# Kernel tuning notes

Hardware: AMD Instinct MI355X
Metric: run time of the kernel (lower is better)

Reference implementation:

```python
import jax, jax.numpy as jnp
import numpy as np

D_IN = 128      # NODE/EDGE_EMBEDDING_SIZE
FC_HID = 512    # FC_HIDDEN_SIZE
FEAT = 256      # GNN_FEAT_SIZE
N1 = 2000; E1 = 2000; N2 = 2000; E2 = 2000
GNN_LAYERS = 3
ALPHA = 200.0   # NORM_ALPHA
BS_ITERS = 10   # BS_ITER_NUM
BS_EPS = 1e-4   # BS_EPSILON


def _l2norm(x, axis=-1, eps=1e-12):
    # torch F.normalize(p=2): x / max(||x||, eps)
    n = jnp.sqrt(jnp.sum(x * x, axis=axis, keepdims=True))
    return x / jnp.maximum(n, eps)


def _pairwise_sim(x, y):
    # s = 1 - cdist(x,y,p=2)/max  on batched [B,N,D],[B,M,D]
    x2 = jnp.sum(x * x, axis=-1)[:, :, None]
    y2 = jnp.sum(y * y, axis=-1)[:, None, :]
    d2 = jnp.maximum(x2 + y2 - 2.0 * jnp.einsum('bnd,bmd->bnm', x, y), 0.0)
    dist = jnp.sqrt(d2)
    return 1.0 - dist / jnp.max(dist)


def _gconv(A, x, w_a, b_a, w_u, b_u):
    # A: [B,N,N]; F.normalize(A, p=1, dim=-2) = column L1 normalization
    An = A / jnp.maximum(jnp.sum(jnp.abs(A), axis=-2, keepdims=True), 1e-12)
    ax = jax.nn.relu(x @ w_a + b_a)
    ux = jax.nn.relu(x @ w_u + b_u)
    return jnp.einsum('bnm,bmd->bnd', An, ax) + ux


def _affinity(X, Y, A):
    S = (A + A.T) * 0.5
    return jnp.einsum('bnd,de,bme->bnm', X, S, Y)


def _sinkhorn(s, n1, n2):
    # nrows/ncols equal full dims in Net.forward, so masks are full blocks.
    NT1, NT2 = s.shape[1], s.shape[2]
    r = jnp.arange(NT1)[:, None]
    c = jnp.arange(NT2)[None, :]
    block = ((r < n1) & (c < n2)) | ((r >= n1) & (c >= n2))
    s = (s + BS_EPS) * block[None].astype(s.dtype)
    for i in range(BS_ITERS):
        if i % 2 == 1:
            s = s / jnp.sum(s, axis=2, keepdims=True)  # row normalization
        else:
            s = s / jnp.sum(s, axis=1, keepdims=True)  # column normalization
    return s


def setup_inputs() -> dict:
    key = jax.random.key(0)
    ks = jax.random.split(key, 22)
    f32 = jnp.float32
    def lin_w(k, din, dout):
        return jax.random.uniform(k, (din, dout), dtype=f32,
                                  minval=-1.0, maxval=1.0) / np.sqrt(din)
    stdv = 1.0 / np.sqrt(FEAT)
    inp = {
        'emb1': jax.random.normal(ks[0], (1, N1, D_IN), dtype=f32),
        'emb2': jax.random.normal(ks[1], (1, N2, D_IN), dtype=f32),
        'edge_emb1': jax.random.normal(ks[2], (1, E1, D_IN), dtype=f32),
        'edge_emb2': jax.random.normal(ks[3], (1, E2, D_IN), dtype=f32),
        'Aidx_src': jax.random.uniform(ks[4], (1, N1 + E1, N1 + E1), dtype=f32),
        'Aidx_tgt': jax.random.uniform(ks[5], (1, N2 + E2, N2 + E2), dtype=f32),
        'fc1n_w': lin_w(ks[6], D_IN, FC_HID), 'fc1n_b': jnp.zeros((FC_HID,), f32),
        'fc2n_w': lin_w(ks[7], FC_HID, FEAT), 'fc2n_b': jnp.zeros((FEAT,), f32),
        'fc1e_w': lin_w(ks[8], D_IN, FC_HID), 'fc1e_b': jnp.zeros((FC_HID,), f32),
        'fc2e_w': lin_w(ks[9], FC_HID, FEAT), 'fc2e_b': jnp.zeros((FEAT,), f32),
        'gnn_a_w': jnp.stack([lin_w(k, FEAT, FEAT) for k in jax.random.split(ks[10], GNN_LAYERS)]),
        'gnn_a_b': jnp.zeros((GNN_LAYERS, FEAT), f32),
        'gnn_u_w': jnp.stack([lin_w(k, FEAT, FEAT) for k in jax.random.split(ks[11], GNN_LAYERS)]),
        'gnn_u_b': jnp.zeros((GNN_LAYERS, FEAT), f32),
        'aff_A': jax.random.uniform(ks[12], (GNN_LAYERS, FEAT, FEAT), dtype=f32,
                                    minval=-stdv, maxval=stdv) + jnp.eye(FEAT, dtype=f32),
        'cg_w': lin_w(ks[13], 2 * FEAT, FEAT), 'cg_b': jnp.zeros((FEAT,), f32),
    }
    return inp


def reference(emb1, emb2, edge_emb1, edge_emb2, Aidx_src, Aidx_tgt,
              fc1n_w, fc1n_b, fc2n_w, fc2n_b, fc1e_w, fc1e_b, fc2e_w, fc2e_b,
              gnn_a_w, gnn_a_b, gnn_u_w, gnn_u_b, aff_A, cg_w, cg_b):
    # node embeddings
    h1 = jax.nn.relu(emb1[0] @ fc1n_w + fc1n_b)
    e1n = _l2norm(h1 @ fc2n_w + fc2n_b)[None]            # [1,N1,FEAT]
    h2 = jax.nn.relu(emb2[0] @ fc1n_w + fc1n_b)
    e2n = _l2norm(h2 @ fc2n_w + fc2n_b)[None]            # [1,N2,FEAT]
    Kp = _pairwise_sim(e1n, e2n)
    # edge embeddings
    g1 = jax.nn.relu(edge_emb1[0] @ fc1e_w + fc1e_b)
    e1e = jax.nn.sigmoid(g1 @ fc2e_w + fc2e_b)[None]     # [1,E1,FEAT]
    g2 = jax.nn.relu(edge_emb2[0] @ fc1e_w + fc1e_b)
    e2e = jax.nn.sigmoid(g2 @ fc2e_w + fc2e_b)[None]     # [1,E2,FEAT]
    Ke = _pairwise_sim(e1e, e2e)

    n1, n2 = e1n.shape[1], e2n.shape[1]
    x1 = jnp.concatenate([e1n, e1e], axis=1)             # [1,N1+E1,FEAT]
    x2 = jnp.concatenate([e2n, e2e], axis=1)
    NT1, NT2 = x1.shape[1], x2.shape[1]

    s = None
    for i in range(GNN_LAYERS):
        x1 = _l2norm(_gconv(Aidx_src, x1, gnn_a_w[i], gnn_a_b[i], gnn_u_w[i], gnn_u_b[i]))
        x2 = _l2norm(_gconv(Aidx_tgt, x2, gnn_a_w[i], gnn_a_b[i], gnn_u_w[i], gnn_u_b[i]))
        s = jnp.zeros((1, NT1, NT2), dtype=x1.dtype)
        s = s.at[:, :n1, :n2].set(_affinity(x1[:, :n1], x2[:, :n2], aff_A[i]))
        s = s.at[:, n1:, n2:].set(_affinity(x1[:, n1:], x2[:, n2:], aff_A[i]))
        s = jax.nn.softmax(ALPHA * s, axis=-1)           # Norm layer
        s = _sinkhorn(s, n1, n2)
        if i == GNN_LAYERS - 2:
            x1n = jnp.concatenate([x1, jnp.einsum('bnm,bmd->bnd', s, x2)], axis=-1) @ cg_w + cg_b
            x2n = jnp.concatenate([x2, jnp.einsum('bnm,bnd->bmd', s, x1)], axis=-1) @ cg_w + cg_b
            x1, x2 = x1n, x2n
    return (s, Kp, Ke)
```

## Files before the change

kernel.cpp:

```cpp
#include <hip/hip_runtime.h>
#include <hip/hip_bf16.h>
#include <math.h>
#include <stdint.h>

typedef __hip_bfloat16 bf16;

#define NN 2000
#define NT 4000
#define FEAT 256
#define FC_HID 512
#define D_IN 128
#define ALPHA_C 200.0f
#define BS_EPS_C 1e-4f
#define SABLK 4000000

__device__ __forceinline__ float ldv_dt(const void* p, size_t i, int dt)
{
    return dt ? __bfloat162float(((const bf16*)p)[i]) : ((const float*)p)[i];
}
__device__ __forceinline__ void stv_dt(void* p, size_t i, float v, int dt)
{
    if (dt) ((bf16*)p)[i] = __float2bfloat16(v);
    else    ((float*)p)[i] = v;
}
__device__ __forceinline__ short f2bf(float f)
{
    bf16 h = __float2bfloat16(f);
    short s; __builtin_memcpy(&s, &h, 2); return s;
}
__device__ __forceinline__ float bfbits2f(uint32_t u16)
{
    uint32_t x = u16 << 16; float f; __builtin_memcpy(&f, &x, 4); return f;
}

__device__ __forceinline__ void swizzle_tiles(int& tx, int& ty, int& tz)
{
    int gx = gridDim.x, gy = gridDim.y, gz = gridDim.z;
    int nwg = gx * gy * gz;
    int flat = ((int)blockIdx.z * gy + (int)blockIdx.y) * gx + (int)blockIdx.x;
    int q = nwg >> 3, r = nwg & 7;
    int xcd = flat & 7, s = flat >> 3;
    int mn = xcd < r ? xcd : r;
    int g = xcd * q + mn + s;
    tx = g % gx;
    int gg = g / gx;
    ty = gg % gy;
    tz = gg / gy;
}

__global__ __launch_bounds__(256) void detect_kernel(const uint32_t* __restrict__ emb,
                                                     int* __restrict__ flag)
{
    int tid = threadIdx.x;
    int cnt = 0;
    for (int i = tid; i < 1024; i += 256) {
        uint32_t e = (emb[i] >> 7) & 0xFF;
        if (e >= 0x30 && e <= 0x44) cnt++;
    }
    for (int o = 32; o; o >>= 1) cnt += __shfl_down(cnt, o);
    __shared__ int red[4];
    if ((tid & 63) == 0) red[tid >> 6] = cnt;
    __syncthreads();
    if (tid == 0) *flag = (red[0] + red[1] + red[2] + red[3] > 512) ? 1 : 0;
}

__global__ void telemetry_kernel(uint32_t* out, uint32_t pattern) { out[0] = pattern; }

__global__ __launch_bounds__(256) void transpose_bf16_kernel(
    const void* __restrict__ in, int mode, size_t off, short* __restrict__ out,
    int R, int C, int ld, const float* __restrict__ rowscale, const int* __restrict__ dtp)
{
    const int dt = mode ? *dtp : 0;
    __shared__ short tl[64][65];
    const int t = threadIdx.x, tx = t & 63, ty = t >> 6;
    const int r0 = blockIdx.y * 64, c0 = blockIdx.x * 64;
    const int gc = c0 + tx;
    for (int i = ty; i < 64; i += 4) {
        int gr = r0 + i;
        float v = 0.f;
        if (gr < R && gc < C) {
            v = ldv_dt(in, off + (size_t)gr * ld + gc, dt);
            if (rowscale) v *= rowscale[gr];
        }
        tl[tx][i] = f2bf(v);
    }
    __syncthreads();
    const int gr2 = r0 + tx;
    for (int i = ty; i < 64; i += 4) {
        int gcc = c0 + i;
        if (gcc < C && gr2 < R) out[(size_t)gcc * R + gr2] = tl[i][tx];
    }
}

__global__ __launch_bounds__(256) void transpose_split_kernel(
    const void* __restrict__ in, int mode, size_t off,
    short* __restrict__ outhi, short* __restrict__ outlo,
    int R, int C, const int* __restrict__ dtp)
{
    const int dt = mode ? *dtp : 0;
    __shared__ float tl[64][65];
    const int t = threadIdx.x, tx = t & 63, ty = t >> 6;
    const int r0 = blockIdx.y * 64, c0 = blockIdx.x * 64;
    const int gc = c0 + tx;
    for (int i = ty; i < 64; i += 4) {
        int gr = r0 + i;
        float v = 0.f;
        if (gr < R && gc < C) v = ldv_dt(in, off + (size_t)gr * C + gc, dt);
        tl[tx][i] = v;
    }
    __syncthreads();
    const int gr2 = r0 + tx;
    for (int i = ty; i < 64; i += 4) {
        int gcc = c0 + i;
        if (gcc < C && gr2 < R) {
            float v = tl[i][tx];
            short h = f2bf(v);
            outhi[(size_t)gcc * R + gr2] = h;
            outlo[(size_t)gcc * R + gr2] = f2bf(v - bfbits2f((uint32_t)(uint16_t)h));
        }
    }
}

__global__ __launch_bounds__(256) void concat_bias_kernel(
    const void* __restrict__ a_b, const void* __restrict__ u_b, size_t bo,
    float* __restrict__ out, const int* __restrict__ dtp)
{
    int j = threadIdx.x, dt = *dtp;
    out[j] = ldv_dt(a_b, bo + j, dt);
    out[256 + j] = ldv_dt(u_b, bo + j, dt);
}

typedef __attribute__((ext_vector_type(8))) short bf16x8;
typedef __attribute__((ext_vector_type(4))) float floatx4;
#define LDST 40
#define LDSROW 80

template <int ATR>
__global__ __launch_bounds__(256) void mfma_gemm(
    const void* __restrict__ A, int amode, size_t a_off,
    const void* __restrict__ B, int bmode, size_t b_off,
    float* __restrict__ C, int M, int N, int K, int lda, int ldb, int ldc,
    const void* __restrict__ bias, size_t bias_off, int bias_dt,
    const float* __restrict__ rowscale, const float* __restrict__ addsrc, int ldadd,
    int epi, const int* __restrict__ dtp)
{
    __shared__ short Als[64][LDSROW];
    __shared__ short Bls[64][LDSROW];
    const int dtf = *dtp;
    const int aet = amode ? dtf : 0;
    const int bet = (bmode == 2) ? 1 : (bmode == 1 ? dtf : 0);
    const int bdt = bias_dt ? dtf : 0;
    const int t = threadIdx.x;
    int bx, by, bz;
    swizzle_tiles(bx, by, bz);
    const int m0 = by * 64;
    const int n0 = bx * 64;
    const int nz = gridDim.z;
    int zlo = 0, zhi = K;
    if (nz > 1) {
        int kb = ((K + nz * 64 - 1) / (nz * 64)) * 64;
        zlo = bz * kb;
        zhi = zlo + kb < K ? zlo + kb : K;
        if (zlo > K) zlo = K;
    }
    const int w = t >> 6, lane = t & 63, quad = lane >> 4, l16 = lane & 15;

    floatx4 acc[4] = {};

    for (int k0 = zlo; k0 < zhi; k0 += 64) {
        const int kk = (t & 3) * 8;
#pragma unroll
        for (int h = 0; h < 2; ++h) {
            const bool hv = (k0 + h * 32) < zhi;
            const int gk = k0 + h * 32 + kk;
            if (ATR == 0) {
                int m = t >> 2;
                int gm = m0 + m;
                short* dst = &Als[m][h * LDST + kk];
                if (hv && gm < M && gk + 8 <= K) {
                    if (aet) {
                        *(uint4*)dst = *(const uint4*)((const ushort*)A + a_off + (size_t)gm * lda + gk);
                    } else {
                        const float* p = (const float*)A + a_off + (size_t)gm * lda + gk;
                        float4 r0 = *(const float4*)p, r1 = *(const float4*)(p + 4);
                        short loc[8];
                        loc[0] = f2bf(r0.x); loc[1] = f2bf(r0.y);
                        loc[2] = f2bf(r0.z); loc[3] = f2bf(r0.w);
                        loc[4] = f2bf(r1.x); loc[5] = f2bf(r1.y);
                        loc[6] = f2bf(r1.z); loc[7] = f2bf(r1.w);
                        *(bf16x8*)dst = *(bf16x8*)loc;
                    }
                } else {
                    short loc[8];
#pragma unroll
                    for (int j = 0; j < 8; ++j) {
                        float v = 0.f;
                        if (hv && gm < M && gk + j < K)
                            v = ldv_dt(A, a_off + (size_t)gm * lda + gk + j, aet);
                        loc[j] = f2bf(v);
                    }
                    *(bf16x8*)dst = *(bf16x8*)loc;
                }
            } else {
                int m = t >> 2;
                int gm = m0 + m;
                short loc[8];
#pragma unroll
                for (int j = 0; j < 8; ++j) {
                    int gkj = gk + j;
                    float v = (hv && gm < M && gkj < K)
                                  ? ((const float*)A)[a_off + (size_t)gkj * lda + gm] : 0.f;
                    loc[j] = f2bf(v);
                }
                *(bf16x8*)&Als[t >> 2][h * LDST + kk] = *(bf16x8*)loc;
            }
            {
                int n = t >> 2;
                int gn = n0 + n;
                short* dst = &Bls[n][h * LDST + kk];
                if (hv && gn < N && gk + 8 <= K) {
                    if (bet) {
                        *(uint4*)dst = *(const uint4*)((const ushort*)B + b_off + (size_t)gn * ldb + gk);
                    } else {
                        const float* p = (const float*)B + b_off + (size_t)gn * ldb + gk;
                        float4 r0 = *(const float4*)p, r1 = *(const float4*)(p + 4);
                        short loc[8];
                        loc[0] = f2bf(r0.x); loc[1] = f2bf(r0.y);
                        loc[2] = f2bf(r0.z); loc[3] = f2bf(r0.w);
                        loc[4] = f2bf(r1.x); loc[5] = f2bf(r1.y);
                        loc[6] = f2bf(r1.z); loc[7] = f2bf(r1.w);
                        *(bf16x8*)dst = *(bf16x8*)loc;
                    }
                } else {
                    short loc[8];
#pragma unroll
                    for (int j = 0; j < 8; ++j) {
                        float v = (hv && gn < N && gk + j < K)
                                      ? ldv_dt(B, b_off + (size_t)gn * ldb + gk + j, bet) : 0.f;
                        loc[j] = f2bf(v);
                    }
                    *(bf16x8*)dst = *(bf16x8*)loc;
                }
            }
        }
        __syncthreads();
#pragma unroll
        for (int h = 0; h < 2; ++h) {
            bf16x8 a = *(const bf16x8*)&Als[w * 16 + l16][h * LDST + quad * 8];
#pragma unroll
            for (int fb = 0; fb < 4; ++fb) {
                bf16x8 b = *(const bf16x8*)&Bls[fb * 16 + l16][h * LDST + quad * 8];
                acc[fb] = __builtin_amdgcn_mfma_f32_16x16x32_bf16(a, b, acc[fb], 0, 0, 0);
            }
        }
        __syncthreads();
    }
    const bool atom = (nz > 1);
#pragma unroll
    for (int fb = 0; fb < 4; ++fb) {
        int gc = n0 + fb * 16 + l16;
        if (gc >= N) continue;
        float bv = (!atom && bias) ? ldv_dt(bias, bias_off + gc, bdt) : 0.f;
#pragma unroll
        for (int r = 0; r < 4; ++r) {
            int gr = m0 + w * 16 + quad * 4 + r;
            if (gr >= M) continue;
            float v = acc[fb][r];
            if (atom) {
                if (rowscale) v *= rowscale[gr];
                atomicAdd(&C[(size_t)gr * ldc + gc], v);
            } else {
                v += bv;
                if (epi == 1) v = fmaxf(v, 0.f);
                else if (epi == 2) v = 1.f / (1.f + expf(-v));
                if (rowscale) v *= rowscale[gr];
                if (addsrc) v += addsrc[(size_t)gr * ldadd + gc];
                C[(size_t)gr * ldc + gc] = v;
            }
        }
    }
}

template <int ATR>
__global__ __launch_bounds__(256) void mfma_gemm2(
    const void* __restrict__ A0, const void* __restrict__ A1, int amode,
    const void* __restrict__ B, int bmode, size_t b_off0, size_t b_off1,
    float* __restrict__ C0, float* __restrict__ C1,
    int M, int N, int K, int lda, int ldb, int ldc,
    const float* __restrict__ rs0, const float* __restrict__ rs1,
    const int* __restrict__ dtp)
{
    __shared__ short Als[64][LDSROW];
    __shared__ short Bls[64][LDSROW];
    const int dtf = *dtp;
    const int aet = amode ? dtf : 0;
    const int bet = (bmode == 2) ? 1 : (bmode == 1 ? dtf : 0);
    const int t = threadIdx.x;
    int bx, by, bz;
    swizzle_tiles(bx, by, bz);
    const int tilesY = (M + 63) >> 6;
    const int half = (by >= tilesY) ? 1 : 0;
    const int m0 = (by - half * tilesY) * 64;
    const int n0 = bx * 64;
    const void* A = half ? A1 : A0;
    float* C = half ? C1 : C0;
    const size_t b_off = half ? b_off1 : b_off0;
    const float* rowscale = half ? rs1 : rs0;
    const int nz = gridDim.z;
    int zlo = 0, zhi = K;
    if (nz > 1) {
        int kb = ((K + nz * 64 - 1) / (nz * 64)) * 64;
        zlo = bz * kb;
        zhi = zlo + kb < K ? zlo + kb : K;
        if (zlo > K) zlo = K;
    }
    const int w = t >> 6, lane = t & 63, quad = lane >> 4, l16 = lane & 15;

    floatx4 acc[4] = {};

    for (int k0 = zlo; k0 < zhi; k0 += 64) {
        const int kk = (t & 3) * 8;
#pragma unroll
        for (int h = 0; h < 2; ++h) {
            const bool hv = (k0 + h * 32) < zhi;
            const int gk = k0 + h * 32 + kk;
            if (ATR == 0) {
                int m = t >> 2;
                int gm = m0 + m;
                short* dst = &Als[m][h * LDST + kk];
                if (hv && gm < M && gk + 8 <= K) {
                    if (aet) {
                        *(uint4*)dst = *(const uint4*)((const ushort*)A + (size_t)gm * lda + gk);
                    } else {
                        const float* p = (const float*)A + (size_t)gm * lda + gk;
                        float4 r0 = *(const float4*)p, r1 = *(const float4*)(p + 4);
                        short loc[8];
                        loc[0] = f2bf(r0.x); loc[1] = f2bf(r0.y);
                        loc[2] = f2bf(r0.z); loc[3] = f2bf(r0.w);
                        loc[4] = f2bf(r1.x); loc[5] = f2bf(r1.y);
                        loc[6] = f2bf(r1.z); loc[7] = f2bf(r1.w);
                        *(bf16x8*)dst = *(bf16x8*)loc;
                    }
                } else {
                    short loc[8];
#pragma unroll
                    for (int j = 0; j < 8; ++j) {
                        float v = 0.f;
                        if (hv && gm < M && gk + j < K)
                            v = ldv_dt(A, (size_t)gm * lda + gk + j, aet);
                        loc[j] = f2bf(v);
                    }
                    *(bf16x8*)dst = *(bf16x8*)loc;
                }
            } else {
                int m = t >> 2;
                int gm = m0 + m;
                short loc[8];
#pragma unroll
                for (int j = 0; j < 8; ++j) {
                    int gkj = gk + j;
                    float v = (hv && gm < M && gkj < K)
                                  ? ((const float*)A)[(size_t)gkj * lda + gm] : 0.f;
                    loc[j] = f2bf(v);
                }
                *(bf16x8*)&Als[t >> 2][h * LDST + kk] = *(bf16x8*)loc;
            }
            {
                int n = t >> 2;
                int gn = n0 + n;
                short* dst = &Bls[n][h * LDST + kk];
                if (hv && gn < N && gk + 8 <= K) {
                    if (bet) {
                        *(uint4*)dst = *(const uint4*)((const ushort*)B + b_off + (size_t)gn * ldb + gk);
                    } else {
                        const float* p = (const float*)B + b_off + (size_t)gn * ldb + gk;
                        float4 r0 = *(const float4*)p, r1 = *(const float4*)(p + 4);
                        short loc[8];
                        loc[0] = f2bf(r0.x); loc[1] = f2bf(r0.y);
                        loc[2] = f2bf(r0.z); loc[3] = f2bf(r0.w);
                        loc[4] = f2bf(r1.x); loc[5] = f2bf(r1.y);
                        loc[6] = f2bf(r1.z); loc[7] = f2bf(r1.w);
                        *(bf16x8*)dst = *(bf16x8*)loc;
                    }
                } else {
                    short loc[8];
#pragma unroll
                    for (int j = 0; j < 8; ++j) {
                        float v = (hv && gn < N && gk + j < K)
                                      ? ldv_dt(B, b_off + (size_t)gn * ldb + gk + j, bet) : 0.f;
                        loc[j] = f2bf(v);
                    }
                    *(bf16x8*)dst = *(bf16x8*)loc;
                }
            }
        }
        __syncthreads();
#pragma unroll
        for (int h = 0; h < 2; ++h) {
            bf16x8 a = *(const bf16x8*)&Als[w * 16 + l16][h * LDST + quad * 8];
#pragma unroll
            for (int fb = 0; fb < 4; ++fb) {
                bf16x8 b = *(const bf16x8*)&Bls[fb * 16 + l16][h * LDST + quad * 8];
                acc[fb] = __builtin_amdgcn_mfma_f32_16x16x32_bf16(a, b, acc[fb], 0, 0, 0);
            }
        }
        __syncthreads();
    }
    const bool atom = (nz > 1);
#pragma unroll
    for (int fb = 0; fb < 4; ++fb) {
        int gc = n0 + fb * 16 + l16;
        if (gc >= N) continue;
#pragma unroll
        for (int r = 0; r < 4; ++r) {
            int gr = m0 + w * 16 + quad * 4 + r;
            if (gr >= M) continue;
            float v = acc[fb][r];
            if (rowscale) v *= rowscale[gr];
            if (atom) atomicAdd(&C[(size_t)gr * ldc + gc], v);
            else      C[(size_t)gr * ldc + gc] = v;
        }
    }
}

__global__ __launch_bounds__(256) void mfma_gemm_split(
    const float* __restrict__ A, const float* __restrict__ B, float* __restrict__ C,
    int M, int N, int K)
{
    __shared__ short Ahi[64][LDST];
    __shared__ short Alo[64][LDST];
    __shared__ short Bhi[64][LDST];
    __shared__ short Blo[64][LDST];
    const int t = threadIdx.x;
    int bx, by, bz;
    swizzle_tiles(bx, by, bz);
    const int m0 = by * 64;
    const int n0 = bx * 64;
    const int w = t >> 6, lane = t & 63, quad = lane >> 4, l16 = lane & 15;

    floatx4 acc[4] = {};

    for (int k0 = 0; k0 < K; k0 += 32) {
        {
            int r = t >> 2, kk = (t & 3) * 8;
            int gm = m0 + r, gk = k0 + kk;
            float v[8] = {};
            if (gm < M) {
                const float* p = A + (size_t)gm * K + gk;
                float4 r0 = *(const float4*)p, r1 = *(const float4*)(p + 4);
                v[0] = r0.x; v[1] = r0.y; v[2] = r0.z; v[3] = r0.w;
                v[4] = r1.x; v[5] = r1.y; v[6] = r1.z; v[7] = r1.w;
            }
            short lh[8], ll[8];
#pragma unroll
            for (int j = 0; j < 8; ++j) {
                short h = f2bf(v[j]);
                lh[j] = h;
                ll[j] = f2bf(v[j] - bfbits2f((uint32_t)(uint16_t)h));
            }
            *(bf16x8*)&Ahi[r][kk] = *(bf16x8*)lh;
            *(bf16x8*)&Alo[r][kk] = *(bf16x8*)ll;
        }
        {
            int r = t >> 2, kk = (t & 3) * 8;
            int gn = n0 + r, gk = k0 + kk;
            float v[8] = {};
            if (gn < N) {
                const float* p = B + (size_t)gn * K + gk;
                float4 r0 = *(const float4*)p, r1 = *(const float4*)(p + 4);
                v[0] = r0.x; v[1] = r0.y; v[2] = r0.z; v[3] = r0.w;
                v[4] = r1.x; v[5] = r1.y; v[6] = r1.z; v[7] = r1.w;
            }
            short lh[8], ll[8];
#pragma unroll
            for (int j = 0; j < 8; ++j) {
                short h = f2bf(v[j]);
                lh[j] = h;
                ll[j] = f2bf(v[j] - bfbits2f((uint32_t)(uint16_t)h));
            }
            *(bf16x8*)&Bhi[r][kk] = *(bf16x8*)lh;
            *(bf16x8*)&Blo[r][kk] = *(bf16x8*)ll;
        }
        __syncthreads();
        bf16x8 ah = *(const bf16x8*)&Ahi[w * 16 + l16][quad * 8];
        bf16x8 al = *(const bf16x8*)&Alo[w * 16 + l16][quad * 8];
#pragma unroll
        for (int fb = 0; fb < 4; ++fb) {
            bf16x8 bh = *(const bf16x8*)&Bhi[fb * 16 + l16][quad * 8];
            bf16x8 bl = *(const bf16x8*)&Blo[fb * 16 + l16][quad * 8];
            acc[fb] = __builtin_amdgcn_mfma_f32_16x16x32_bf16(ah, bh, acc[fb], 0, 0, 0);
            acc[fb] = __builtin_amdgcn_mfma_f32_16x16x32_bf16(al, bh, acc[fb], 0, 0, 0);
            acc[fb] = __builtin_amdgcn_mfma_f32_16x16x32_bf16(ah, bl, acc[fb], 0, 0, 0);
        }
        __syncthreads();
    }
#pragma unroll
    for (int fb = 0; fb < 4; ++fb) {
        int gc = n0 + fb * 16 + l16;
        if (gc >= N) continue;
#pragma unroll
        for (int r = 0; r < 4; ++r) {
            int gr = m0 + w * 16 + quad * 4 + r;
            if (gr >= M) continue;
            C[(size_t)gr * N + gc] = acc[fb][r];
        }
    }
}

__global__ __launch_bounds__(256) void mfma_mlp_split(
    const void* __restrict__ A, int amode,
    const short* __restrict__ Whi, const short* __restrict__ Wlo,
    float* __restrict__ C, int M, int N, int K, int ldc,
    const void* __restrict__ bias, int epi, const int* __restrict__ dtp)
{
    __shared__ short Ahi[64][LDST];
    __shared__ short Alo[64][LDST];
    __shared__ short Bh[64][LDST];
    __shared__ short Bl[64][LDST];
    const int dtf = *dtp;
    const int aet = amode ? dtf : 0;
    const int t = threadIdx.x;
    int bx, by, bz;
    swizzle_tiles(bx, by, bz);
    const int m0 = by * 64;
    const int n0 = bx * 64;
    const int w = t >> 6, lane = t & 63, quad = lane >> 4, l16 = lane & 15;

    floatx4 acc[4] = {};

    for (int k0 = 0; k0 < K; k0 += 32) {
        {
            int r = t >> 2, kk = (t & 3) * 8;
            int gm = m0 + r, gk = k0 + kk;
            float v[8] = {};
            if (gm < M) {
                if (aet) {
                    uint4 raw = *(const uint4*)((const ushort*)A + (size_t)gm * K + gk);
                    uint32_t uu[4] = {raw.x, raw.y, raw.z, raw.w};
#pragma unroll
                    for (int q = 0; q < 4; ++q) {
                        v[2 * q]     = bfbits2f(uu[q] & 0xFFFFu);
                        v[2 * q + 1] = bfbits2f(uu[q] >> 16);
                    }
                } else {
                    const float* p = (const float*)A + (size_t)gm * K + gk;
                    float4 r0 = *(const float4*)p, r1 = *(const float4*)(p + 4);
                    v[0] = r0.x; v[1] = r0.y; v[2] = r0.z; v[3] = r0.w;
                    v[4] = r1.x; v[5] = r1.y; v[6] = r1.z; v[7] = r1.w;
                }
            }
            short lh[8], ll[8];
#pragma unroll
            for (int j = 0; j < 8; ++j) {
                short h = f2bf(v[j]);
                lh[j] = h;
                ll[j] = f2bf(v[j] - bfbits2f((uint32_t)(uint16_t)h));
            }
            *(bf16x8*)&Ahi[r][kk] = *(bf16x8*)lh;
            *(bf16x8*)&Alo[r][kk] = *(bf16x8*)ll;
        }
        {
            int n = t >> 2, kk = (t & 3) * 8;
            int gn = n0 + n, gk = k0 + kk;
            if (gn < N) {
                *(uint4*)&Bh[n][kk] = *(const uint4*)&Whi[(size_t)gn * K + gk];
                *(uint4*)&Bl[n][kk] = *(const uint4*)&Wlo[(size_t)gn * K + gk];
            } else {
                short z[8] = {};
                *(bf16x8*)&Bh[n][kk] = *(bf16x8*)z;
                *(bf16x8*)&Bl[n][kk] = *(bf16x8*)z;
            }
        }
        __syncthreads();
        bf16x8 ah = *(const bf16x8*)&Ahi[w * 16 + l16][quad * 8];
        bf16x8 al = *(const bf16x8*)&Alo[w * 16 + l16][quad * 8];
#pragma unroll
        for (int fb = 0; fb < 4; ++fb) {
            bf16x8 bh = *(const bf16x8*)&Bh[fb * 16 + l16][quad * 8];
            bf16x8 bl = *(const bf16x8*)&Bl[fb * 16 + l16][quad * 8];
            acc[fb] = __builtin_amdgcn_mfma_f32_16x16x32_bf16(ah, bh, acc[fb], 0, 0, 0);
            acc[fb] = __builtin_amdgcn_mfma_f32_16x16x32_bf16(al, bh, acc[fb], 0, 0, 0);
            acc[fb] = __builtin_amdgcn_mfma_f32_16x16x32_bf16(ah, bl, acc[fb], 0, 0, 0);
        }
        __syncthreads();
    }
#pragma unroll
    for (int fb = 0; fb < 4; ++fb) {
        int gc = n0 + fb * 16 + l16;
        if (gc >= N) continue;
        float bv = bias ? ldv_dt(bias, gc, *dtp) : 0.f;
#pragma unroll
        for (int r = 0; r < 4; ++r) {
            int gr = m0 + w * 16 + quad * 4 + r;
            if (gr >= M) continue;
            float v = acc[fb][r] + bv;
            if (epi == 1) v = fmaxf(v, 0.f);
            else if (epi == 2) v = 1.f / (1.f + expf(-v));
            C[(size_t)gr * ldc + gc] = v;
        }
    }
}

__global__ void fill_kernel(float* p, float v, int n)
{
    int i = blockIdx.x * 256 + threadIdx.x;
    if (i < n) p[i] = v;
}

__global__ __launch_bounds__(256) void l2norm_kernel(const float* __restrict__ src,
                                                     int lds, float* __restrict__ dst)
{
    int row = blockIdx.x, tid = threadIdx.x;
    float v = src[(size_t)row * lds + tid];
    float s = v * v;
    for (int o = 32; o; o >>= 1) s += __shfl_down(s, o);
    __shared__ float red[4];
    if ((tid & 63) == 0) red[tid >> 6] = s;
    __syncthreads();
    float tot = red[0] + red[1] + red[2] + red[3];
    float scale = 1.f / fmaxf(sqrtf(tot), 1e-12f);
    dst[(size_t)row * FEAT + tid] = v * scale;
}

__global__ __launch_bounds__(256) void rownorm2_kernel(const float* __restrict__ src,
                                                       float* __restrict__ out)
{
    int row = blockIdx.x, tid = threadIdx.x;
    float v = src[(size_t)row * FEAT + tid];
    float s = v * v;
    for (int o = 32; o; o >>= 1) s += __shfl_down(s, o);
    __shared__ float red[4];
    if ((tid & 63) == 0) red[tid >> 6] = s;
    __syncthreads();
    if (tid == 0) out[row] = red[0] + red[1] + red[2] + red[3];
}

__global__ __launch_bounds__(256) void d2max_rows_kernel(const float* __restrict__ G,
                                                         const float* __restrict__ x2,
                                                         const float* __restrict__ y2,
                                                         float* __restrict__ rowmax)
{
    int i = blockIdx.x, tid = threadIdx.x;
    float xi = x2[i];
    const float* Gr = G + (size_t)i * NN;
    float m = 0.f;
    for (int j = tid; j < NN; j += 256)
        m = fmaxf(m, xi + y2[j] - 2.f * Gr[j]);
    for (int o = 32; o; o >>= 1) m = fmaxf(m, __shfl_down(m, o));
    __shared__ float red[4];
    if ((tid & 63) == 0) red[tid >> 6] = m;
    __syncthreads();
    if (tid == 0) rowmax[i] = fmaxf(fmaxf(red[0], red[1]), fmaxf(red[2], red[3]));
}

__global__ __launch_bounds__(256) void maxreduce_kernel(const float* __restrict__ rowmax,
                                                        float* __restrict__ gmax, int n)
{
    int tid = threadIdx.x;
    float m = 0.f;
    for (int i = tid; i < n; i += 256) m = fmaxf(m, rowmax[i]);
    for (int o = 32; o; o >>= 1) m = fmaxf(m, __shfl_down(m, o));
    __shared__ float red[4];
    if ((tid & 63) == 0) red[tid >> 6] = m;
    __syncthreads();
    if (tid == 0) *gmax = sqrtf(fmaxf(fmaxf(fmaxf(red[0], red[1]),
                                            fmaxf(red[2], red[3])), 0.f));
}

__global__ __launch_bounds__(256) void pw_out_kernel(void* __restrict__ out, size_t elem_off,
                                                     const float* __restrict__ G,
                                                     const float* __restrict__ x2,
                                                     const float* __restrict__ y2,
                                                     const float* __restrict__ gmax,
                                                     const int* __restrict__ dtp)
{
    int j = blockIdx.x * 256 + threadIdx.x;
    int i = blockIdx.y;
    if (j >= NN) return;
    float inv = 1.f / *gmax;
    float d2 = fmaxf(x2[i] + y2[j] - 2.f * G[(size_t)i * NN + j], 0.f);
    stv_dt(out, elem_off + (size_t)i * NN + j, 1.f - sqrtf(d2) * inv, *dtp);
}

__global__ __launch_bounds__(256) void colsum_kernel(const void* __restrict__ A0,
                                                     const void* __restrict__ A1,
                                                     float* __restrict__ out,
                                                     const int* __restrict__ dtp)
{
    const void* A = blockIdx.z ? A1 : A0;
    int dt = *dtp;
    int col = blockIdx.x * 256 + threadIdx.x;
    if (col >= NT) return;
    int r0 = blockIdx.y * 100;
    float s = 0.f;
#pragma unroll 4
    for (int r = r0; r < r0 + 100; ++r) s += fabsf(ldv_dt(A, (size_t)r * NT + col, dt));
    atomicAdd(&out[blockIdx.z * NT + col], s);
}

__global__ void recipclamp_kernel(float* p, int n)
{
    int i = blockIdx.x * 256 + threadIdx.x;
    if (i < n) p[i] = 1.f / fmaxf(p[i], 1e-12f);
}

__global__ __launch_bounds__(256) void symavg_kernel(const void* __restrict__ A,
                                                     size_t a_off,
                                                     float* __restrict__ S,
                                                     const int* __restrict__ dtp)
{
    int dt = *dtp;
    int i = blockIdx.x, j = threadIdx.x;
    S[i * 256 + j] = 0.5f * (ldv_dt(A, a_off + i * 256 + j, dt) +
                             ldv_dt(A, a_off + j * 256 + i, dt));
}

__global__ __launch_bounds__(256) void softmax_stats_kernel(const float* __restrict__ Sa,
                                                            float* __restrict__ ms,
                                                            float* __restrict__ dinv)
{
    int row = blockIdx.x, z = blockIdx.z, tid = threadIdx.x;
    const float* Srow = Sa + (size_t)z * SABLK + (size_t)row * NN;
    __shared__ float red[4];
    float m = 0.f;
    for (int j = tid; j < NN; j += 256) m = fmaxf(m, ALPHA_C * Srow[j]);
    for (int o = 32; o; o >>= 1) m = fmaxf(m, __shfl_down(m, o));
    if ((tid & 63) == 0) red[tid >> 6] = m;
    __syncthreads();
    m = fmaxf(fmaxf(red[0], red[1]), fmaxf(red[2], red[3]));
    __syncthreads();
    float s = 0.f;
    for (int j = tid; j < NN; j += 256) s += expf(ALPHA_C * Srow[j] - m);
    for (int o = 32; o; o >>= 1) s += __shfl_down(s, o);
    if ((tid & 63) == 0) red[tid >> 6] = s;
    __syncthreads();
    if (tid == 0) {
        float tot = red[0] + red[1] + red[2] + red[3] + (float)NN * expf(-m);
        ms[z * NN + row] = m;
        dinv[z * NN + row] = 1.f / tot;
    }
}

__global__ __launch_bounds__(256) void exp_transform_kernel(float* __restrict__ Sa,
                                                            const float* __restrict__ ms,
                                                            const float* __restrict__ dinv)
{
    int z = blockIdx.z, row = blockIdx.y;
    int idx = blockIdx.x * 256 + threadIdx.x;
    if (idx >= 500) return;
    float m = ms[z * NN + row], dv = dinv[z * NN + row];
    float4* p = (float4*)(Sa + (size_t)z * SABLK + (size_t)row * NN) + idx;
    float4 v = *p;
    v.x = expf(ALPHA_C * v.x - m) * dv + BS_EPS_C;
    v.y = expf(ALPHA_C * v.y - m) * dv + BS_EPS_C;
    v.z = expf(ALPHA_C * v.z - m) * dv + BS_EPS_C;
    v.w = expf(ALPHA_C * v.w - m) * dv + BS_EPS_C;
    *p = v;
}

__global__ __launch_bounds__(256) void colmv_partial_kernel(const float* __restrict__ E,
                                                            const float* __restrict__ vec,
                                                            float* __restrict__ partial)
{
    int col = blockIdx.x * 256 + threadIdx.x;
    int z = blockIdx.z;
    if (col >= NN) return;
    int r0 = blockIdx.y * 50;
    const float* Eb = E + (size_t)z * SABLK;
    const float* v = vec ? vec + z * NN : nullptr;
    float s = 0.f;
    for (int r = r0; r < r0 + 50; ++r) {
        float e = Eb[(size_t)r * NN + col];
        s += v ? e * v[r] : e;
    }
    atomicAdd(&partial[z * NN + col], s);
}

__global__ void recip_vec_kernel(const float* __restrict__ in, float* __restrict__ out, int n)
{
    int i = blockIdx.x * 256 + threadIdx.x;
    if (i < n) out[i] = 1.f / in[i];
}

__global__ __launch_bounds__(256) void rowmv_kernel(const float* __restrict__ E,
                                                    const float* __restrict__ vec,
                                                    float* __restrict__ out)
{
    int row = blockIdx.x, z = blockIdx.z, tid = threadIdx.x;
    const float* Er = E + (size_t)z * SABLK + (size_t)row * NN;
    const float* v = vec + z * NN;
    float s = 0.f;
    for (int j = tid; j < NN; j += 256) s += Er[j] * v[j];
    for (int o = 32; o; o >>= 1) s += __shfl_down(s, o);
    __shared__ float red[4];
    if ((tid & 63) == 0) red[tid >> 6] = s;
    __syncthreads();
    if (tid == 0) out[z * NN + row] = 1.f / (red[0] + red[1] + red[2] + red[3]);
}

__global__ __launch_bounds__(256) void writes_kernel(void* __restrict__ out,
                                                     const float* __restrict__ E,
                                                     const float* __restrict__ rvec,
                                                     const float* __restrict__ cvec,
                                                     const int* __restrict__ dtp)
{
    int i = blockIdx.x, tid = threadIdx.x;
    int dt = *dtp;
    int z = (i < NN) ? 0 : 1;
    int r = z ? i - NN : i;
    const float* Erow = E + (size_t)z * SABLK + (size_t)r * NN;
    float rv = rvec[i];
    for (int j = tid; j < NT; j += 256) {
        float v = 0.f;
        bool inblk = z ? (j >= NN) : (j < NN);
        if (inblk) {
            int jj = z ? (j - NN) : j;
            v = rv * Erow[jj] * cvec[j];
            if (!(v == v) || fabsf(v) > 1e30f) v = 0.f;
        }
        stv_dt(out, (size_t)i * NT + j, v, dt);
    }
}

extern "C" void kernel_launch(void* const* d_in, const int* in_sizes, int n_in,
                              void* d_out, int out_size, void* d_ws, size_t ws_size,
                              hipStream_t stream)
{
    (void)in_sizes; (void)n_in; (void)out_size;
    const void* emb1   = d_in[0];
    const void* emb2   = d_in[1];
    const void* eemb1  = d_in[2];
    const void* eemb2  = d_in[3];
    const void* Asrc   = d_in[4];
    const void* Atgt   = d_in[5];
    const void* fc1n_w = d_in[6];
    const void* fc1n_b = d_in[7];
    const void* fc2n_w = d_in[8];
    const void* fc2n_b = d_in[9];
    const void* fc1e_w = d_in[10];
    const void* fc1e_b = d_in[11];
    const void* fc2e_w = d_in[12];
    const void* fc2e_b = d_in[13];
    const void* gnn_a_w = d_in[14];
    const void* gnn_a_b = d_in[15];
    const void* gnn_u_w = d_in[16];
    const void* gnn_u_b = d_in[17];
    const void* aff_A  = d_in[18];
    const void* cg_w   = d_in[19];
    const void* cg_b   = d_in[20];

    const size_t KP_OFF = 16000000;
    const size_t KE_OFF = 20000000;

    const size_t NEED = 50808960;
    if (ws_size < NEED) {
        float tv = 10000.f + (float)(ws_size >> 20);
        bf16 tb = __float2bfloat16(tv);
        uint16_t tbits; __builtin_memcpy(&tbits, &tb, 2);
        uint32_t pattern = ((uint32_t)tbits << 16) | tbits;
        telemetry_kernel<<<1, 1, 0, stream>>>((uint32_t*)d_out, pattern);
        return;
    }
    char* Wb = (char*)d_ws;
    size_t off = 0;
    auto allocf = [&](size_t n) { float* p = (float*)(Wb + off); off += n * 4; return p; };
    float* x1     = allocf(1024000);
    float* x2     = allocf(1024000);
    float* ax     = allocf(1024000);
    float* ux     = allocf(1024000);
    float* XS     = allocf(512000);
    float* Ssym   = allocf(65536);
    float* colsum = allocf(8192);
    float* rn2a   = allocf(2048);
    float* rn2b   = allocf(2048);
    float* rvec   = allocf(4096);
    float* cvec   = allocf(4096);
    float* ms     = allocf(4096);
    float* dinv   = allocf(4096);
    float* gmax   = allocf(16);
    int*   dtp    = (int*)allocf(16);
    float* Sa     = allocf(8000000);
    float* G      = Sa;
    float* tmpx1  = Sa;
    float* tmpx2  = Sa + 1024000;
    float* h      = ax;
    float* partial = XS;
    float* XS2    = ax;
    short* wuT    = (short*)(Sa + 2100000);
    float* bias512 = Sa + 2200000;
    float* axu_b  = Sa + 2300000;
    short* axT_b  = (short*)(Sa + 6450000);
    short* cgT    = (short*)Ssym;
    short* XST    = (short*)XS;
    short* w1hiT = (short*)Sa;
    short* w1loT = w1hiT + FC_HID * D_IN;
    short* w2hiT = w1loT + FC_HID * D_IN;
    short* w2loT = w2hiT + FEAT * FC_HID;

    dim3 B(256);
    auto g2 = [](int M, int N) { return dim3((N + 63) / 64, (M + 63) / 64); };
    auto gb2 = [](int Mh, int N, int nz) {
        return dim3((N + 63) / 64, 2 * ((Mh + 63) / 64), nz);
    };
    auto gt = [](int R, int C) { return dim3((C + 63) / 64, (R + 63) / 64); };
    const float* NF = nullptr;
    const void* NV = nullptr;

    detect_kernel<<<1, B, 0, stream>>>((const uint32_t*)emb1, dtp);

    struct { const void* e; const void* w1; const void* b1; const void* w2;
             const void* b2; float* dst; int epi; } mlp[4] = {
        {emb1,  fc1n_w, fc1n_b, fc2n_w, fc2n_b, x1,          0},
        {emb2,  fc1n_w, fc1n_b, fc2n_w, fc2n_b, x2,          0},
        {eemb1, fc1e_w, fc1e_b, fc2e_w, fc2e_b, x1 + 512000, 2},
        {eemb2, fc1e_w, fc1e_b, fc2e_w, fc2e_b, x2 + 512000, 2},
    };
    for (int m = 0; m < 4; ++m) {
        if (m == 0 || m == 2) {
            transpose_split_kernel<<<gt(D_IN, FC_HID), B, 0, stream>>>(
                mlp[m].w1, 1, 0, w1hiT, w1loT, D_IN, FC_HID, dtp);
            transpose_split_kernel<<<gt(FC_HID, FEAT), B, 0, stream>>>(
                mlp[m].w2, 1, 0, w2hiT, w2loT, FC_HID, FEAT, dtp);
        }
        mfma_mlp_split<<<g2(NN, FC_HID), B, 0, stream>>>(
            mlp[m].e, 1, w1hiT, w1loT, h, NN, FC_HID, D_IN, FC_HID,
            mlp[m].b1, 1, dtp);
        mfma_mlp_split<<<g2(NN, FEAT), B, 0, stream>>>(
            h, 0, w2hiT, w2loT, mlp[m].dst, NN, FEAT, FC_HID, FEAT,
            mlp[m].b2, mlp[m].epi, dtp);
        if (mlp[m].epi == 0)
            l2norm_kernel<<<NN, B, 0, stream>>>(mlp[m].dst, FEAT, mlp[m].dst);
    }

    for (int e = 0; e < 2; ++e) {
        const float* a = e ? x1 + 512000 : x1;
        const float* b = e ? x2 + 512000 : x2;
        size_t oeo = e ? KE_OFF : KP_OFF;
        rownorm2_kernel<<<NN, B, 0, stream>>>(a, rn2a);
        rownorm2_kernel<<<NN, B, 0, stream>>>(b, rn2b);
        mfma_gemm_split<<<g2(NN, NN), B, 0, stream>>>(a, b, G, NN, NN, FEAT);
        d2max_rows_kernel<<<NN, B, 0, stream>>>(G, rn2a, rn2b, partial);
        maxreduce_kernel<<<1, B, 0, stream>>>(partial, gmax, NN);
        pw_out_kernel<<<dim3(8, NN), B, 0, stream>>>(d_out, oeo, G, rn2a, rn2b, gmax, dtp);
    }

    fill_kernel<<<(8192 + 255) / 256, B, 0, stream>>>(colsum, 0.f, 8192);
    colsum_kernel<<<dim3(16, 40, 2), B, 0, stream>>>(Asrc, Atgt, colsum, dtp);
    recipclamp_kernel<<<(8000 + 255) / 256, B, 0, stream>>>(colsum, 8000);

    float* src1 = x1;
    for (int i = 0; i < 3; ++i) {
        size_t wo = (size_t)i * 65536, bo = (size_t)i * 256;
        transpose_bf16_kernel<<<gt(256, 256), B, 0, stream>>>(
            gnn_a_w, 1, wo, wuT, 256, 256, 256, NF, dtp);
        transpose_bf16_kernel<<<gt(256, 256), B, 0, stream>>>(
            gnn_u_w, 1, wo, wuT + 65536, 256, 256, 256, NF, dtp);
        concat_bias_kernel<<<1, B, 0, stream>>>(gnn_a_b, gnn_u_b, bo, bias512, dtp);
        mfma_gemm<0><<<g2(2 * NT, 512), B, 0, stream>>>(
            src1, 0, 0, wuT, 2, 0, axu_b, 2 * NT, 512, FEAT, FEAT, FEAT, 512,
            bias512, 0, 0, NF, NF, 0, 1, dtp);
        transpose_bf16_kernel<<<gt(2 * NT, 256), B, 0, stream>>>(
            axu_b, 0, 0, axT_b, 2 * NT, 256, 512, colsum, dtp);
        mfma_gemm2<0><<<gb2(NT, FEAT, 8), B, 0, stream>>>(
            Asrc, Atgt, 1, axT_b, 2, 0, NT,
            axu_b + 256, axu_b + (size_t)NT * 512 + 256,
            NT, FEAT, NT, NT, 2 * NT, 512, NF, NF, dtp);
        l2norm_kernel<<<2 * NT, B, 0, stream>>>(axu_b + 256, 512, x1);
        src1 = x1;
        if (i >= 1) {
            symavg_kernel<<<256, B, 0, stream>>>(aff_A, (size_t)i * 65536, Ssym, dtp);
            mfma_gemm<0><<<g2(2 * NN, FEAT), B, 0, stream>>>(
                x1, 0, 0, Ssym, 0, 0, XS2, 2 * NN, FEAT, FEAT, FEAT, FEAT, FEAT,
                NV, 0, 0, NF, NF, 0, 0, dtp);
            mfma_gemm2<0><<<gb2(NN, NN, 1), B, 0, stream>>>(
                XS2, XS2 + 512000, 0, x2, 0, 0, 512000,
                Sa, Sa + SABLK, NN, NN, FEAT, FEAT, FEAT, NN, NF, NF, dtp);
            softmax_stats_kernel<<<dim3(NN, 1, 2), B, 0, stream>>>(Sa, ms, dinv);
            exp_transform_kernel<<<dim3(2, NN, 2), B, 0, stream>>>(Sa, ms, dinv);
            for (int t = 0; t < 10; ++t) {
                if ((t & 1) == 0) {
                    fill_kernel<<<16, B, 0, stream>>>(partial, 0.f, 4096);
                    colmv_partial_kernel<<<dim3(8, 40, 2), B, 0, stream>>>(
                        Sa, t == 0 ? NF : rvec, partial);
                    recip_vec_kernel<<<16, B, 0, stream>>>(partial, cvec, 4000);
                } else {
                    rowmv_kernel<<<dim3(NN, 1, 2), B, 0, stream>>>(Sa, cvec, rvec);
                }
            }
            if (i == 1) {
                fill_kernel<<<8000, B, 0, stream>>>(ax, 0.f, 2048000);
                transpose_bf16_kernel<<<gt(2 * NN, 256), B, 0, stream>>>(
                    x2, 0, 0, XST, 2 * NN, 256, 256, cvec, dtp);
                mfma_gemm2<0><<<gb2(NN, FEAT, 8), B, 0, stream>>>(
                    Sa, Sa + SABLK, 0, XST, 2, 0, NN,
                    ax, ax + 512000, NN, FEAT, NN, NN, 2 * NN, FEAT,
                    rvec, rvec + NN, dtp);
                transpose_bf16_kernel<<<gt(2 * NN, 256), B, 0, stream>>>(
                    x1, 0, 0, XST, 2 * NN, 256, 256, rvec, dtp);
                mfma_gemm2<1><<<gb2(NN, FEAT, 8), B, 0, stream>>>(
                    Sa, Sa + SABLK, 0, XST, 2, 0, NN,
                    ux, ux + 512000, NN, FEAT, NN, NN, 2 * NN, FEAT,
                    cvec, cvec + NN, dtp);
                transpose_bf16_kernel<<<gt(512, 256), B, 0, stream>>>(
                    cg_w, 1, 0, cgT, 512, 256, 256, NF, dtp);
                mfma_gemm<0><<<g2(2 * NT, FEAT), B, 0, stream>>>(
                    x1, 0, 0, cgT, 2, 0, tmpx1, 2 * NT, FEAT, FEAT, FEAT, 512, FEAT,
                    cg_b, 0, 1, NF, NF, 0, 0, dtp);
                mfma_gemm<0><<<g2(2 * NT, FEAT), B, 0, stream>>>(
                    ax, 0, 0, cgT, 2, 256, tmpx1, 2 * NT, FEAT, FEAT, FEAT, 512, FEAT,
                    NV, 0, 0, NF, tmpx1, FEAT, 0, dtp);
                src1 = tmpx1;
            }
            if (i == 2) {
                writes_kernel<<<NT, B, 0, stream>>>(d_out, Sa, rvec, cvec, dtp);
            }
        }
    }
}
```

Measured before the change: 1.425 ms.

## Batch paired MLP and pairwise-distance launches, halve split-K factor

The two MLP passes for each graph pair now run in one launch each, and both node and edge pairwise-similarity pipelines (gram GEMM, row-max, reduce, output) are merged into single z-batched launches. This cuts launch count and fills the GPU better, since each 2000-row problem alone occupies few tiles. The split-K factor for the big A·x and S·x GEMMs drops from 8 to 4, which reduces atomic traffic but lowers parallelism. The atomic-mode flag now comes from gridDim.z. Buffers were reassigned (ax for the hidden layer, rvec/cvec for norms, Sa for both grams), so any aliasing mistake could corrupt results.

```diff
diff --git a/kernel.cpp b/kernel.cpp
--- a/kernel.cpp
+++ b/kernel.cpp
@@ -13,6 +13,8 @@
 #define ALPHA_C 200.0f
 #define BS_EPS_C 1e-4f
 #define SABLK 4000000
+#define KP_OFF_C 16000000
+#define KE_OFF_C 20000000
 
 __device__ __forceinline__ float ldv_dt(const void* p, size_t i, int dt)
 {
@@ -255,7 +257,7 @@
         }
         __syncthreads();
     }
-    const bool atom = (nz > 1);
+    const bool atom = (gridDim.z > 1);
 #pragma unroll
     for (int fb = 0; fb < 4; ++fb) {
         int gc = n0 + fb * 16 + l16;
@@ -406,7 +408,7 @@
         }
         __syncthreads();
     }
-    const bool atom = (nz > 1);
+    const bool atom = (gridDim.z > 1);
 #pragma unroll
     for (int fb = 0; fb < 4; ++fb) {
         int gc = n0 + fb * 16 + l16;
@@ -423,8 +425,10 @@
     }
 }
 
-__global__ __launch_bounds__(256) void mfma_gemm_split(
-    const float* __restrict__ A, const float* __restrict__ B, float* __restrict__ C,
+__global__ __launch_bounds__(256) void mfma_gemm_split2(
+    const float* __restrict__ A0, const float* __restrict__ A1,
+    const float* __restrict__ B0, const float* __restrict__ B1,
+    float* __restrict__ C0, float* __restrict__ C1,
     int M, int N, int K)
 {
     __shared__ short Ahi[64][LDST];
@@ -434,8 +438,13 @@
     const int t = threadIdx.x;
     int bx, by, bz;
     swizzle_tiles(bx, by, bz);
-    const int m0 = by * 64;
+    const int tilesY = (M + 63) >> 6;
+    const int half = (by >= tilesY) ? 1 : 0;
+    const int m0 = (by - half * tilesY) * 64;
     const int n0 = bx * 64;
+    const float* A = half ? A1 : A0;
+    const float* Bp = half ? B1 : B0;
+    float* C = half ? C1 : C0;
     const int w = t >> 6, lane = t & 63, quad = lane >> 4, l16 = lane & 15;
 
     floatx4 acc[4] = {};
@@ -466,7 +475,7 @@
             int gn = n0 + r, gk = k0 + kk;
             float v[8] = {};
             if (gn < N) {
-                const float* p = B + (size_t)gn * K + gk;
+                const float* p = Bp + (size_t)gn * K + gk;
                 float4 r0 = *(const float4*)p, r1 = *(const float4*)(p + 4);
                 v[0] = r0.x; v[1] = r0.y; v[2] = r0.z; v[3] = r0.w;
                 v[4] = r1.x; v[5] = r1.y; v[6] = r1.z; v[7] = r1.w;
@@ -507,10 +516,11 @@
     }
 }
 
-__global__ __launch_bounds__(256) void mfma_mlp_split(
-    const void* __restrict__ A, int amode,
+__global__ __launch_bounds__(256) void mfma_mlp_split2(
+    const void* __restrict__ A0, const void* __restrict__ A1, int amode,
     const short* __restrict__ Whi, const short* __restrict__ Wlo,
-    float* __restrict__ C, int M, int N, int K, int ldc,
+    float* __restrict__ C0, float* __restrict__ C1,
+    int M, int N, int K, int ldc,
     const void* __restrict__ bias, int epi, const int* __restrict__ dtp)
 {
     __shared__ short Ahi[64][LDST];
@@ -522,8 +532,12 @@
     const int t = threadIdx.x;
     int bx, by, bz;
     swizzle_tiles(bx, by, bz);
-    const int m0 = by * 64;
+    const int tilesY = (M + 63) >> 6;
+    const int half = (by >= tilesY) ? 1 : 0;
+    const int m0 = (by - half * tilesY) * 64;
     const int n0 = bx * 64;
+    const void* A = half ? A1 : A0;
+    float* C = half ? C1 : C0;
     const int w = t >> 6, lane = t & 63, quad = lane >> 4, l16 = lane & 15;
 
     floatx4 acc[4] = {};
@@ -635,13 +649,15 @@
     if (tid == 0) out[row] = red[0] + red[1] + red[2] + red[3];
 }
 
-__global__ __launch_bounds__(256) void d2max_rows_kernel(const float* __restrict__ G,
-                                                         const float* __restrict__ x2,
-                                                         const float* __restrict__ y2,
+__global__ __launch_bounds__(256) void d2max_rows_kernel(const float* __restrict__ Gb,
+                                                         const float* __restrict__ rnA,
+                                                         const float* __restrict__ rnB,
                                                          float* __restrict__ rowmax)
 {
-    int i = blockIdx.x, tid = threadIdx.x;
-    float xi = x2[i];
+    int i = blockIdx.x, z = blockIdx.z, tid = threadIdx.x;
+    const float* G = Gb + (size_t)z * SABLK;
+    float xi = rnA[z * NN + i];
+    const float* y2 = rnB + z * NN;
     const float* Gr = G + (size_t)i * NN;
     float m = 0.f;
     for (int j = tid; j < NN; j += 256)
@@ -650,35 +666,38 @@
     __shared__ float red[4];
     if ((tid & 63) == 0) red[tid >> 6] = m;
     __syncthreads();
-    if (tid == 0) rowmax[i] = fmaxf(fmaxf(red[0], red[1]), fmaxf(red[2], red[3]));
+    if (tid == 0) rowmax[z * 2048 + i] = fmaxf(fmaxf(red[0], red[1]), fmaxf(red[2], red[3]));
 }
 
 __global__ __launch_bounds__(256) void maxreduce_kernel(const float* __restrict__ rowmax,
                                                         float* __restrict__ gmax, int n)
 {
-    int tid = threadIdx.x;
+    int tid = threadIdx.x, z = blockIdx.z;
+    const float* rm = rowmax + z * 2048;
     float m = 0.f;
-    for (int i = tid; i < n; i += 256) m = fmaxf(m, rowmax[i]);
+    for (int i = tid; i < n; i += 256) m = fmaxf(m, rm[i]);
     for (int o = 32; o; o >>= 1) m = fmaxf(m, __shfl_down(m, o));
     __shared__ float red[4];
     if ((tid & 63) == 0) red[tid >> 6] = m;
     __syncthreads();
-    if (tid == 0) *gmax = sqrtf(fmaxf(fmaxf(fmaxf(red[0], red[1]),
-                                            fmaxf(red[2], red[3])), 0.f));
-}
-
-__global__ __launch_bounds__(256) void pw_out_kernel(void* __restrict__ out, size_t elem_off,
-                                                     const float* __restrict__ G,
-                                                     const float* __restrict__ x2,
-                                                     const float* __restrict__ y2,
+    if (tid == 0) gmax[z] = sqrtf(fmaxf(fmaxf(fmaxf(red[0], red[1]),
+                                              fmaxf(red[2], red[3])), 0.f));
+}
+
+__global__ __launch_bounds__(256) void pw_out_kernel(void* __restrict__ out,
+                                                     const float* __restrict__ Gb,
+                                                     const float* __restrict__ rnA,
+                                                     const float* __restrict__ rnB,
                                                      const float* __restrict__ gmax,
                                                      const int* __restrict__ dtp)
 {
     int j = blockIdx.x * 256 + threadIdx.x;
-    int i = blockIdx.y;
+    int i = blockIdx.y, z = blockIdx.z;
     if (j >= NN) return;
-    float inv = 1.f / *gmax;
-    float d2 = fmaxf(x2[i] + y2[j] - 2.f * G[(size_t)i * NN + j], 0.f);
+    size_t elem_off = z ? KE_OFF_C : KP_OFF_C;
+    const float* G = Gb + (size_t)z * SABLK;
+    float inv = 1.f / gmax[z];
+    float d2 = fmaxf(rnA[z * NN + i] + rnB[z * NN + j] - 2.f * G[(size_t)i * NN + j], 0.f);
     stv_dt(out, elem_off + (size_t)i * NN + j, 1.f - sqrtf(d2) * inv, *dtp);
 }
 
@@ -849,9 +868,6 @@
     const void* cg_w   = d_in[19];
     const void* cg_b   = d_in[20];
 
-    const size_t KP_OFF = 16000000;
-    const size_t KE_OFF = 20000000;
-
     const size_t NEED = 50808960;
     if (ws_size < NEED) {
         float tv = 10000.f + (float)(ws_size >> 20);
@@ -880,10 +896,8 @@
     float* gmax   = allocf(16);
     int*   dtp    = (int*)allocf(16);
     float* Sa     = allocf(8000000);
-    float* G      = Sa;
     float* tmpx1  = Sa;
     float* tmpx2  = Sa + 1024000;
-    float* h      = ax;
     float* partial = XS;
     float* XS2    = ax;
     short* wuT    = (short*)(Sa + 2100000);
@@ -908,41 +922,35 @@
 
     detect_kernel<<<1, B, 0, stream>>>((const uint32_t*)emb1, dtp);
 
-    struct { const void* e; const void* w1; const void* b1; const void* w2;
-             const void* b2; float* dst; int epi; } mlp[4] = {
-        {emb1,  fc1n_w, fc1n_b, fc2n_w, fc2n_b, x1,          0},
-        {emb2,  fc1n_w, fc1n_b, fc2n_w, fc2n_b, x2,          0},
-        {eemb1, fc1e_w, fc1e_b, fc2e_w, fc2e_b, x1 + 512000, 2},
-        {eemb2, fc1e_w, fc1e_b, fc2e_w, fc2e_b, x2 + 512000, 2},
+    struct { const void* e0; const void* e1; const void* w1; const void* b1;
+             const void* w2; const void* b2; float* d0; float* d1; int epi; } mp[2] = {
+        {emb1,  emb2,  fc1n_w, fc1n_b, fc2n_w, fc2n_b, x1,          x2,          0},
+        {eemb1, eemb2, fc1e_w, fc1e_b, fc2e_w, fc2e_b, x1 + 512000, x2 + 512000, 2},
     };
-    for (int m = 0; m < 4; ++m) {
-        if (m == 0 || m == 2) {
-            transpose_split_kernel<<<gt(D_IN, FC_HID), B, 0, stream>>>(
-                mlp[m].w1, 1, 0, w1hiT, w1loT, D_IN, FC_HID, dtp);
-            transpose_split_kernel<<<gt(FC_HID, FEAT), B, 0, stream>>>(
-                mlp[m].w2, 1, 0, w2hiT, w2loT, FC_HID, FEAT, dtp);
-        }
-        mfma_mlp_split<<<g2(NN, FC_HID), B, 0, stream>>>(
-            mlp[m].e, 1, w1hiT, w1loT, h, NN, FC_HID, D_IN, FC_HID,
-            mlp[m].b1, 1, dtp);
-        mfma_mlp_split<<<g2(NN, FEAT), B, 0, stream>>>(
-            h, 0, w2hiT, w2loT, mlp[m].dst, NN, FEAT, FC_HID, FEAT,
-            mlp[m].b2, mlp[m].epi, dtp);
-        if (mlp[m].epi == 0)
-            l2norm_kernel<<<NN, B, 0, stream>>>(mlp[m].dst, FEAT, mlp[m].dst);
-    }
-
-    for (int e = 0; e < 2; ++e) {
-        const float* a = e ? x1 + 512000 : x1;
-        const float* b = e ? x2 + 512000 : x2;
-        size_t oeo = e ? KE_OFF : KP_OFF;
-        rownorm2_kernel<<<NN, B, 0, stream>>>(a, rn2a);
-        rownorm2_kernel<<<NN, B, 0, stream>>>(b, rn2b);
-        mfma_gemm_split<<<g2(NN, NN), B, 0, stream>>>(a, b, G, NN, NN, FEAT);
-        d2max_rows_kernel<<<NN, B, 0, stream>>>(G, rn2a, rn2b, partial);
-        maxreduce_kernel<<<1, B, 0, stream>>>(partial, gmax, NN);
-        pw_out_kernel<<<dim3(8, NN), B, 0, stream>>>(d_out, oeo, G, rn2a, rn2b, gmax, dtp);
-    }
+    for (int p = 0; p < 2; ++p) {
+        transpose_split_kernel<<<gt(D_IN, FC_HID), B, 0, stream>>>(
+            mp[p].w1, 1, 0, w1hiT, w1loT, D_IN, FC_HID, dtp);
+        transpose_split_kernel<<<gt(FC_HID, FEAT), B, 0, stream>>>(
+            mp[p].w2, 1, 0, w2hiT, w2loT, FC_HID, FEAT, dtp);
+        mfma_mlp_split2<<<gb2(NN, FC_HID, 1), B, 0, stream>>>(
+            mp[p].e0, mp[p].e1, 1, w1hiT, w1loT, ax, ax + 1024000,
+            NN, FC_HID, D_IN, FC_HID, mp[p].b1, 1, dtp);
+        mfma_mlp_split2<<<gb2(NN, FEAT, 1), B, 0, stream>>>(
+            ax, ax + 1024000, 0, w2hiT, w2loT, mp[p].d0, mp[p].d1,
+            NN, FEAT, FC_HID, FEAT, mp[p].b2, mp[p].epi, dtp);
+        if (mp[p].epi == 0) {
+            l2norm_kernel<<<NN, B, 0, stream>>>(mp[p].d0, FEAT, mp[p].d0);
+            l2norm_kernel<<<NN, B, 0, stream>>>(mp[p].d1, FEAT, mp[p].d1);
+        }
+    }
+
+    rownorm2_kernel<<<2 * NN, B, 0, stream>>>(x1, rvec);
+    rownorm2_kernel<<<2 * NN, B, 0, stream>>>(x2, cvec);
+    mfma_gemm_split2<<<gb2(NN, NN, 1), B, 0, stream>>>(
+        x1, x1 + 512000, x2, x2 + 512000, Sa, Sa + SABLK, NN, NN, FEAT);
+    d2max_rows_kernel<<<dim3(NN, 1, 2), B, 0, stream>>>(Sa, rvec, cvec, partial);
+    maxreduce_kernel<<<dim3(1, 1, 2), B, 0, stream>>>(partial, gmax, NN);
+    pw_out_kernel<<<dim3(8, NN, 2), B, 0, stream>>>(d_out, Sa, rvec, cvec, gmax, dtp);
 
     fill_kernel<<<(8192 + 255) / 256, B, 0, stream>>>(colsum, 0.f, 8192);
     colsum_kernel<<<dim3(16, 40, 2), B, 0, stream>>>(Asrc, Atgt, colsum, dtp);
@@ -961,7 +969,7 @@
             bias512, 0, 0, NF, NF, 0, 1, dtp);
         transpose_bf16_kernel<<<gt(2 * NT, 256), B, 0, stream>>>(
             axu_b, 0, 0, axT_b, 2 * NT, 256, 512, colsum, dtp);
-        mfma_gemm2<0><<<gb2(NT, FEAT, 8), B, 0, stream>>>(
+        mfma_gemm2<0><<<gb2(NT, FEAT, 4), B, 0, stream>>>(
             Asrc, Atgt, 1, axT_b, 2, 0, NT,
             axu_b + 256, axu_b + (size_t)NT * 512 + 256,
             NT, FEAT, NT, NT, 2 * NT, 512, NF, NF, dtp);
@@ -991,13 +999,13 @@
                 fill_kernel<<<8000, B, 0, stream>>>(ax, 0.f, 2048000);
                 transpose_bf16_kernel<<<gt(2 * NN, 256), B, 0, stream>>>(
                     x2, 0, 0, XST, 2 * NN, 256, 256, cvec, dtp);
-                mfma_gemm2<0><<<gb2(NN, FEAT, 8), B, 0, stream>>>(
+                mfma_gemm2<0><<<gb2(NN, FEAT, 4), B, 0, stream>>>(
                     Sa, Sa + SABLK, 0, XST, 2, 0, NN,
                     ax, ax + 512000, NN, FEAT, NN, NN, 2 * NN, FEAT,
                     rvec, rvec + NN, dtp);
                 transpose_bf16_kernel<<<gt(2 * NN, 256), B, 0, stream>>>(
                     x1, 0, 0, XST, 2 * NN, 256, 256, rvec, dtp);
-                mfma_gemm2<1><<<gb2(NN, FEAT, 8), B, 0, stream>>>(
+                mfma_gemm2<1><<<gb2(NN, FEAT, 4), B, 0, stream>>>(
                     Sa, Sa + SABLK, 0, XST, 2, 0, NN,
                     ux, ux + 512000, NN, FEAT, NN, NN, 2 * NN, FEAT,
                     cvec, cvec + NN, dtp);
@@ -1016,4 +1024,5 @@
             }
         }
     }
-}
+    (void)rn2a; (void)rn2b; (void)tmpx2;
+}
```

New measurement: 1.308 ms. 8.2% less time.
